# Kernel tuning notes

Measured on AMD Instinct MI355X. Metric: run time of the kernel, lower is better.

Reference implementation:

```python
import jax, jax.numpy as jnp
import numpy as np

N, C_IN, H, W = 16, 32, 512, 512
C_OUT, K, STRIDE = 32, 3, 1


def setup_inputs() -> dict:
    key = jax.random.key(0)
    k1, k2, k3 = jax.random.split(key, 3)
    x = jax.random.normal(k1, (N, C_IN, H, W), dtype=jnp.float32)
    weight = jax.random.normal(k2, (C_OUT, C_IN, K, K), dtype=jnp.float32) * 0.05
    bias = jax.random.normal(k3, (C_OUT,), dtype=jnp.float32) * 0.05
    return {"x": x, "weight": weight, "bias": bias}


def reference(x, weight, bias):
    # Direct 2D convolution, NCHW / OIHW, stride 1, no padding (VALID),
    # matching the module's per-pixel multiply+sum with padding=0.
    out = jax.lax.conv_general_dilated(
        x, weight,
        window_strides=(STRIDE, STRIDE),
        padding="VALID",
        dimension_numbers=("NCHW", "OIHW", "NCHW"),
    )
    return out + bias[None, :, None, None]
```

## Files before the change

### kernel.cpp

```cpp
#include <hip/hip_runtime.h>


namespace {
constexpr int NI    = 16;
constexpr int C_IN  = 32;
constexpr int HI    = 512;
constexpr int WI    = 512;
constexpr int C_OUT = 32;
constexpr int HO    = 510;
constexpr int WO    = 510;

constexpr int RT    = 6;
constexpr int PT    = 256;
constexpr int XCOLS = 264;
constexpr int PSTR  = 36;
constexpr int SLOTS = 3;
constexpr int SLOTW = XCOLS * PSTR;
constexpr int HIWI  = HI * WI;
constexpr int NT    = 512;
}

typedef __attribute__((ext_vector_type(4))) float  floatx4;
typedef __attribute__((ext_vector_type(8))) __bf16 bf16x8;
typedef __attribute__((ext_vector_type(4))) __bf16 bf16x4;

__global__ void conv_wprep(const float* __restrict__ w, __bf16* __restrict__ ws) {
  const int t = threadIdx.x;
  for (int i = t; i < 9 * 2 * 64 * 8; i += 256) {
    const int j    = i & 7;
    const int lane = (i >> 3) & 63;
    const int h    = (i >> 9) & 1;
    const int tap  = i >> 10;
    const int co   = h * 16 + (lane & 15);
    const int ci   = (lane >> 4) * 8 + j;
    ws[i] = (__bf16)w[(co * C_IN + ci) * 9 + tap];
  }
}

__global__ __launch_bounds__(NT, 4)
void conv3x3_mfma(const float* __restrict__ x, const __bf16* __restrict__ ws,
                  const float* __restrict__ bias, float* __restrict__ out) {
  __shared__ __bf16 lds[SLOTS * SLOTW];

  const int t    = threadIdx.x;
  const int lane = t & 63;
  const int wv   = t >> 6;
  const int quad = lane >> 4;
  const int l16  = lane & 15;
  const int ch   = wv >> 2;
  const int wq   = wv & 3;

  const int x0 = blockIdx.x * PT;
  const int y0 = blockIdx.y * RT;
  const int n  = blockIdx.z;

  const float* xb = x + (size_t)n * C_IN * HIWI + (size_t)y0 * WI + x0;

  const int Abase = (wv * 4) * HIWI + lane;
  const int Pbase = lane * PSTR + wv * 4;
  const bool hw  = (t < 256);
  const int hci  = (t >> 3) & 31;
  const int hpx  = 256 + (t & 7);
  const int hgo  = hci * HIWI + ((x0 + hpx <= WI - 1) ? hpx : (WI - 1 - x0));
  const int hlo  = hpx * PSTR + hci;

  float buf[16];
  float hb = 0.f;

  auto issue = [&](int gr) {
    const float* rb = xb + gr * WI;
#pragma unroll
    for (int k = 0; k < 16; ++k)
      buf[k] = rb[Abase + (k >> 2) * HIWI + (k & 3) * 64];
    if (hw) hb = rb[hgo];
  };
  auto commit = [&](int gr) {
    __bf16* s = lds + (gr % SLOTS) * SLOTW;
#pragma unroll
    for (int k = 0; k < 16; ++k)
      s[Pbase + (k & 3) * 64 * PSTR + (k >> 2)] = (__bf16)buf[k];
    if (hw) s[hlo] = (__bf16)hb;
  };

  bf16x8 afrag[9];
  float bv[4];

  issue(0);
#pragma unroll
  for (int tap = 0; tap < 9; ++tap)
    afrag[tap] = *reinterpret_cast<const bf16x8*>(ws + ((tap * 2 + ch) * 64 + lane) * 8);
  commit(0);
  issue(1);
#pragma unroll
  for (int r = 0; r < 4; ++r)
    bv[r] = bias[ch * 16 + quad * 4 + r];
  commit(1);
  issue(2);
  commit(2);

  __syncthreads();

  const int pxb = x0 + wq * 64 + l16;

#pragma unroll
  for (int row = 0; row < RT; ++row) {
    if (row < RT - 1) issue(row + 3);

    floatx4 acc[4];
#pragma unroll
    for (int f = 0; f < 4; ++f)
      acc[f] = floatx4{bv[0], bv[1], bv[2], bv[3]};

#pragma unroll
    for (int ky = 0; ky < 3; ++ky) {
      const __bf16* sl = lds + ((row + ky) % SLOTS) * SLOTW
                       + (wq * 64 + l16) * PSTR + quad * 8;
#pragma unroll
      for (int kx = 0; kx < 3; ++kx)
#pragma unroll
        for (int f = 0; f < 4; ++f) {
          const __bf16* p = sl + (f * 16 + kx) * PSTR;
          union { bf16x8 v; bf16x4 h[2]; } b;
          b.h[0] = *reinterpret_cast<const bf16x4*>(p);
          b.h[1] = *reinterpret_cast<const bf16x4*>(p + 4);
          acc[f] = __builtin_amdgcn_mfma_f32_16x16x32_bf16(afrag[ky * 3 + kx], b.v, acc[f], 0, 0, 0);
        }
    }

    float* op = out + ((size_t)(n * C_OUT + ch * 16 + quad * 4) * HO + (y0 + row)) * WO + pxb;
#pragma unroll
    for (int f = 0; f < 4; ++f) {
      if (pxb + f * 16 < WO) {
#pragma unroll
        for (int r = 0; r < 4; ++r)
          op[r * (HO * WO) + f * 16] = acc[f][r];
      }
    }

    if (row < RT - 1) {
      __syncthreads();
      commit(row + 3);
      __syncthreads();
    }
  }
}

extern "C" void kernel_launch(void* const* d_in, const int* in_sizes, int n_in,
                              void* d_out, int out_size, void* d_ws, size_t ws_size,
                              hipStream_t stream) {
  const float* x    = (const float*)d_in[0];
  const float* w    = (const float*)d_in[1];
  const float* bias = (const float*)d_in[2];
  float* out        = (float*)d_out;
  __bf16* ws        = (__bf16*)d_ws;

  conv_wprep<<<dim3(1), 256, 0, stream>>>(w, ws);

  dim3 grid(WI / PT, HO / RT, NI);
  conv3x3_mfma<<<grid, NT, 0, stream>>>(x, ws, bias, out);
}
```

Baseline: 928.1 us.

## Restructure conv to input-row streaming with rolling accumulators and 1024-thread blocks

The main loop now iterates over input rows instead of output rows. Each loaded LDS row's B fragments are read once and applied to the up to three output rows that use it, with accumulators kept in a rolling set of three. Block size doubles to 1024 threads with 32-pixel-wide waves. LDS staging is repacked so each thread writes 8 channels as a single 16-byte vector, with padded stride 40. The goal is to cut redundant LDS reads and the two barriers per row, at the cost of more accumulator registers and a larger block that may lower occupancy.

Result: faster. 905.0 us (-2.5%).

```diff
diff --git a/kernel.cpp b/kernel.cpp
--- a/kernel.cpp
+++ b/kernel.cpp
@@ -13,16 +13,16 @@
 constexpr int RT    = 6;
 constexpr int PT    = 256;
 constexpr int XCOLS = 264;
-constexpr int PSTR  = 36;
+constexpr int PSTR  = 40;
 constexpr int SLOTS = 3;
 constexpr int SLOTW = XCOLS * PSTR;
 constexpr int HIWI  = HI * WI;
-constexpr int NT    = 512;
+constexpr int NT    = 1024;
 }
 
 typedef __attribute__((ext_vector_type(4))) float  floatx4;
 typedef __attribute__((ext_vector_type(8))) __bf16 bf16x8;
-typedef __attribute__((ext_vector_type(4))) __bf16 bf16x4;
+typedef __attribute__((ext_vector_type(8))) unsigned short ushortx8;
 
 __global__ void conv_wprep(const float* __restrict__ w, __bf16* __restrict__ ws) {
   const int t = threadIdx.x;
@@ -47,101 +47,111 @@
   const int wv   = t >> 6;
   const int quad = lane >> 4;
   const int l16  = lane & 15;
-  const int ch   = wv >> 2;
-  const int wq   = wv & 3;
+  const int ch   = wv >> 3;
+  const int w8   = wv & 7;
 
   const int x0 = blockIdx.x * PT;
   const int y0 = blockIdx.y * RT;
   const int n  = blockIdx.z;
 
-  const float* xb = x + (size_t)n * C_IN * HIWI + (size_t)y0 * WI + x0;
+  const float* xn = x + (size_t)n * C_IN * HIWI;
 
-  const int Abase = (wv * 4) * HIWI + lane;
-  const int Pbase = lane * PSTR + wv * 4;
-  const bool hw  = (t < 256);
-  const int hci  = (t >> 3) & 31;
+  const int ps   = t & 255;
+  const int cq   = t >> 8;
+  const int gofs = (cq * 8) * HIWI + x0 + ps;
+  const int lofs = ps * PSTR + cq * 8;
+
+  const bool hw  = (wv < 4);
+  const int hci  = t >> 3;
   const int hpx  = 256 + (t & 7);
-  const int hgo  = hci * HIWI + ((x0 + hpx <= WI - 1) ? hpx : (WI - 1 - x0));
+  int hgx = x0 + hpx; if (hgx > WI - 1) hgx = WI - 1;
+  const int hgo  = hci * HIWI + hgx;
   const int hlo  = hpx * PSTR + hci;
 
-  float buf[16];
-  float hb = 0.f;
-
-  auto issue = [&](int gr) {
-    const float* rb = xb + gr * WI;
+  auto issue = [&](int gr, float (&b)[8], float& h) {
+    const float* rb = xn + (size_t)(y0 + gr) * WI;
 #pragma unroll
-    for (int k = 0; k < 16; ++k)
-      buf[k] = rb[Abase + (k >> 2) * HIWI + (k & 3) * 64];
-    if (hw) hb = rb[hgo];
+    for (int k = 0; k < 8; ++k) b[k] = rb[gofs + k * HIWI];
+    if (hw) h = rb[hgo];
   };
-  auto commit = [&](int gr) {
-    __bf16* s = lds + (gr % SLOTS) * SLOTW;
+  auto commit = [&](int slot, float (&b)[8], float h) {
+    __bf16* s = lds + slot * SLOTW;
+    union { __bf16 bb[8]; ushortx8 u; } pk;
 #pragma unroll
-    for (int k = 0; k < 16; ++k)
-      s[Pbase + (k & 3) * 64 * PSTR + (k >> 2)] = (__bf16)buf[k];
-    if (hw) s[hlo] = (__bf16)hb;
+    for (int k = 0; k < 8; ++k) pk.bb[k] = (__bf16)b[k];
+    *reinterpret_cast<ushortx8*>(s + lofs) = pk.u;
+    if (hw) s[hlo] = (__bf16)h;
   };
 
+  {
+    float p0[8], p1[8], p2[8];
+    float h0 = 0.f, h1 = 0.f, h2 = 0.f;
+    issue(0, p0, h0); issue(1, p1, h1); issue(2, p2, h2);
+    commit(0, p0, h0); commit(1, p1, h1); commit(2, p2, h2);
+  }
+
   bf16x8 afrag[9];
-  float bv[4];
-
-  issue(0);
 #pragma unroll
   for (int tap = 0; tap < 9; ++tap)
     afrag[tap] = *reinterpret_cast<const bf16x8*>(ws + ((tap * 2 + ch) * 64 + lane) * 8);
-  commit(0);
-  issue(1);
+
+  float bv[4];
 #pragma unroll
   for (int r = 0; r < 4; ++r)
     bv[r] = bias[ch * 16 + quad * 4 + r];
-  commit(1);
-  issue(2);
-  commit(2);
 
   __syncthreads();
 
-  const int pxb = x0 + wq * 64 + l16;
+  const int pxb = x0 + w8 * 32 + l16;
+  floatx4 acc[3][2];
+  float buf[8]; float hb = 0.f;
 
 #pragma unroll
-  for (int row = 0; row < RT; ++row) {
-    if (row < RT - 1) issue(row + 3);
+  for (int ir = 0; ir < RT + 2; ++ir) {
+    if (ir + 3 < RT + 2) issue(ir + 3, buf, hb);
 
-    floatx4 acc[4];
+    if (ir < RT) {
 #pragma unroll
-    for (int f = 0; f < 4; ++f)
-      acc[f] = floatx4{bv[0], bv[1], bv[2], bv[3]};
+      for (int f = 0; f < 2; ++f)
+        acc[ir % 3][f] = floatx4{bv[0], bv[1], bv[2], bv[3]};
+    }
+
+    bf16x8 bf[2][3];
+    const __bf16* sl = lds + (ir % SLOTS) * SLOTW + (w8 * 32 + l16) * PSTR + quad * 8;
+#pragma unroll
+    for (int f = 0; f < 2; ++f)
+#pragma unroll
+      for (int kx = 0; kx < 3; ++kx)
+        bf[f][kx] = *reinterpret_cast<const bf16x8*>(sl + (f * 16 + kx) * PSTR);
 
 #pragma unroll
     for (int ky = 0; ky < 3; ++ky) {
-      const __bf16* sl = lds + ((row + ky) % SLOTS) * SLOTW
-                       + (wq * 64 + l16) * PSTR + quad * 8;
+      const int o = ir - ky;
+      if (o < 0 || o >= RT) continue;
 #pragma unroll
       for (int kx = 0; kx < 3; ++kx)
 #pragma unroll
-        for (int f = 0; f < 4; ++f) {
-          const __bf16* p = sl + (f * 16 + kx) * PSTR;
-          union { bf16x8 v; bf16x4 h[2]; } b;
-          b.h[0] = *reinterpret_cast<const bf16x4*>(p);
-          b.h[1] = *reinterpret_cast<const bf16x4*>(p + 4);
-          acc[f] = __builtin_amdgcn_mfma_f32_16x16x32_bf16(afrag[ky * 3 + kx], b.v, acc[f], 0, 0, 0);
-        }
+        for (int f = 0; f < 2; ++f)
+          acc[o % 3][f] = __builtin_amdgcn_mfma_f32_16x16x32_bf16(
+              afrag[ky * 3 + kx], bf[f][kx], acc[o % 3][f], 0, 0, 0);
     }
 
-    float* op = out + ((size_t)(n * C_OUT + ch * 16 + quad * 4) * HO + (y0 + row)) * WO + pxb;
+    if (ir >= 2) {
+      const int o = ir - 2;
+      float* op = out + ((size_t)(n * C_OUT + ch * 16 + quad * 4) * HO + (y0 + o)) * WO + pxb;
 #pragma unroll
-    for (int f = 0; f < 4; ++f) {
-      if (pxb + f * 16 < WO) {
+      for (int f = 0; f < 2; ++f) {
+        if (pxb + f * 16 < WO) {
 #pragma unroll
-        for (int r = 0; r < 4; ++r)
-          op[r * (HO * WO) + f * 16] = acc[f][r];
+          for (int r = 0; r < 4; ++r)
+            op[r * (HO * WO) + f * 16] = acc[o % 3][f][r];
+        }
       }
     }
 
-    if (row < RT - 1) {
-      __syncthreads();
-      commit(row + 3);
-      __syncthreads();
-    }
+    __syncthreads();
+    if (ir + 3 < RT + 2)
+      commit(ir % SLOTS, buf, hb);
   }
 }
 
```
